# Kernel optimization log

Measured on AMD Instinct MI355X. Metric: run time of the kernel, lower is better.

The kernel has to match this reference:

```python
import jax, jax.numpy as jnp
import numpy as np


def _conv1x1(x, w, b):
    # x: [B, Cin, T, H, W], w: [Cout, Cin], b: [Cout] -> [B, Cout, T, H, W]
    return jnp.einsum('bcthw,oc->bothw', x, w) + b[None, :, None, None, None]


def setup_inputs() -> dict:
    key = jax.random.key(0)
    ks = jax.random.split(key, 9)
    B, Ci, T, H, W = 2, 128, 4, 32, 32
    Co = 64
    s_in = 1.0 / np.sqrt(Ci)
    s_out = 1.0 / np.sqrt(Co)
    return {
        'z': jax.random.normal(ks[0], (B, Ci, T, H, W), dtype=jnp.float32),
        'w_theta': jax.random.uniform(ks[1], (Co, Ci), jnp.float32, -s_in, s_in),
        'b_theta': jax.random.uniform(ks[2], (Co,), jnp.float32, -s_in, s_in),
        'w_phi': jax.random.uniform(ks[3], (Co, Ci), jnp.float32, -s_in, s_in),
        'b_phi': jax.random.uniform(ks[4], (Co,), jnp.float32, -s_in, s_in),
        'w_psi': jax.random.uniform(ks[5], (Co, Ci), jnp.float32, -s_in, s_in),
        'b_psi': jax.random.uniform(ks[6], (Co,), jnp.float32, -s_in, s_in),
        'w_v': jax.random.uniform(ks[7], (Ci, Co), jnp.float32, -s_out, s_out),
        'b_v': jax.random.uniform(ks[8], (Ci,), jnp.float32, -s_out, s_out),
    }


def reference(z, w_theta, b_theta, w_phi, b_phi, w_psi, b_psi, w_v, b_v):
    B, Ci, T, H, W = z.shape
    Co = w_theta.shape[0]
    N = T * H * W
    # 1x1 conv projections, flattened to [B, Co, N]
    theta = _conv1x1(z, w_theta, b_theta).reshape(B, Co, N)
    phi = _conv1x1(z, w_phi, b_phi).reshape(B, Co, N)
    psi = _conv1x1(z, w_psi, b_psi).reshape(B, Co, N)
    # g = phi^T @ psi : [B, N, N]; normalize with ReLU(g / N)
    g = jnp.einsum('bcn,bcm->bnm', phi, psi)
    norm_g = jax.nn.relu(g / jnp.asarray(N, z.dtype))
    # tmp = norm_g @ theta^T -> [B, N, Co] -> [B, Co, T, H, W]
    tmp = jnp.einsum('bnm,bcm->bcn', norm_g, theta).reshape(B, Co, T, H, W)
    vg = _conv1x1(tmp, w_v, b_v)
    return vg + z
```

## Files before the change

### kernel.cpp

```cpp
#include <hip/hip_runtime.h>


#define NSEQ 4096
#define CI 128
#define CO 64

typedef __attribute__((ext_vector_type(8))) short bf16x8;
typedef __attribute__((ext_vector_type(4))) short bf16x4;
typedef __attribute__((ext_vector_type(4))) float f32x4;

static __device__ inline short f2bf(float f) {
  union { float f; unsigned u; } v; v.f = f;
  unsigned r = v.u + 0x7fffu + ((v.u >> 16) & 1u);
  return (short)(r >> 16);
}

__global__ __launch_bounds__(256, 1) void proj_kernel(
    const float* __restrict__ z,
    const float* __restrict__ w_th, const float* __restrict__ b_th,
    const float* __restrict__ w_ph, const float* __restrict__ b_ph,
    const float* __restrict__ w_ps, const float* __restrict__ b_ps,
    short* __restrict__ Qg, short* __restrict__ Kg, short* __restrict__ Vt)
{
  __shared__ f32x4 zt4[16384 / 16];
  char* zt = (char*)zt4;

  const int wgid = blockIdx.x;
  const int b = wgid >> 6;
  const int n0 = (wgid & 63) * 64;
  const int t = threadIdx.x;

  {
    const int ck = t & 15;
    const int cr = t >> 4;
#pragma unroll
    for (int g = 0; g < 8; ++g) {
      const int c = g * 16 + cr;
      f32x4 v = *(const f32x4*)(z + (size_t)(b * CI + c) * NSEQ + n0 + ck * 4);
#pragma unroll
      for (int i = 0; i < 4; ++i) {
        const int n = ck * 4 + i;
        const int chunk = (c >> 3) ^ (n & 7);
        *(short*)(zt + n * 256 + chunk * 16 + (c & 7) * 2) = f2bf(v[i]);
      }
    }
  }
  __syncthreads();

  const int w = t >> 6, l = t & 63, lr = l & 15, lg = l >> 4;
  const int nw = w * 16;
  const f32x4 zero4 = {0.f, 0.f, 0.f, 0.f};

  bf16x8 a[4];
#pragma unroll
  for (int ks = 0; ks < 4; ++ks) {
    const int n = nw + lr;
    const int chunk = (ks * 4 + lg) ^ (n & 7);
    a[ks] = *(const bf16x8*)(zt + n * 256 + chunk * 16);
  }

  const float* Ws[3]   = {w_ph, w_ps, w_th};
  const float* Bias[3] = {b_ph, b_ps, b_th};

#pragma unroll
  for (int mat = 0; mat < 3; ++mat) {
    const float* W = Ws[mat];
#pragma unroll
    for (int osub = 0; osub < 4; ++osub) {
      const int o = osub * 16 + lr;
      f32x4 acc = zero4;
#pragma unroll
      for (int ks = 0; ks < 4; ++ks) {
        const float* wp = W + o * CI + ks * 32 + lg * 8;
        f32x4 x0 = *(const f32x4*)wp;
        f32x4 x1 = *(const f32x4*)(wp + 4);
        bf16x8 bf;
#pragma unroll
        for (int j = 0; j < 4; ++j) { bf[j] = f2bf(x0[j]); bf[4 + j] = f2bf(x1[j]); }
        acc = __builtin_amdgcn_mfma_f32_16x16x32_bf16(a[ks], bf, acc, 0, 0, 0);
      }
      const float bias = Bias[mat][o];
      if (mat == 2) {
        bf16x4 pk;
#pragma unroll
        for (int r = 0; r < 4; ++r) pk[r] = f2bf(acc[r] + bias);
        *(bf16x4*)(Vt + (size_t)(b * CO + o) * NSEQ + n0 + nw + lg * 4) = pk;
      } else {
        short* dst = (mat == 0 ? Qg : Kg) + (size_t)(b * NSEQ + n0 + nw + lg * 4) * CO + o;
#pragma unroll
        for (int r = 0; r < 4; ++r) dst[(size_t)r * CO] = f2bf(acc[r] + bias);
      }
    }
  }
}

__global__ __launch_bounds__(256, 1) void attn_kernel(
    const short* __restrict__ Qg, const short* __restrict__ Kg,
    const short* __restrict__ Vt, const float* __restrict__ w_v,
    const float* __restrict__ b_v, const float* __restrict__ z,
    float* __restrict__ out)
{
  __shared__ f32x4 smem4[40960 / 16];
  char* smem = (char*)smem4;

  const int wg = blockIdx.x;
  const int b = wg >> 7;
  const int nt = wg & 127;
  const int n0 = nt * 32;
  const int t = threadIdx.x;
  const int w = t >> 6;
  const int l = t & 63;
  const int lr = l & 15;
  const int lg = l >> 4;
  const int tw = w >> 1;
  const int nbase = n0 + (w & 1) * 16;
  const f32x4 zero4 = {0.f, 0.f, 0.f, 0.f};

  bf16x8 q0, q1;
  {
    const short* qp = Qg + (size_t)(b * NSEQ + nbase + lr) * CO + lg * 8;
    q0 = *(const bf16x8*)qp;
    q1 = *(const bf16x8*)(qp + 32);
  }

  f32x4 oacc[4];
#pragma unroll
  for (int i = 0; i < 4; ++i) oacc[i] = zero4;

  char* Pb = smem + 32768 + w * 2048;

  bf16x8 stg[8];
  auto load_stage = [&](int ss) {
    const int m0 = ss * 128;
#pragma unroll
    for (int r = 0; r < 8; ++r) {
      const int chunk = r * 256 + w * 64 + l;
      const int row = (chunk >> 3) & 63;
      const int lc = chunk & 7;
      const short* src;
      if (r < 4) {
        const int m = m0 + (chunk >> 9) * 64 + row;
        src = Kg + (size_t)(b * NSEQ + m) * CO + lc * 8;
      } else {
        src = Vt + (size_t)(b * CO + row) * NSEQ + m0 + ((chunk >> 9) - 2) * 64 + lc * 8;
      }
      stg[r] = *(const bf16x8*)src;
    }
  };
  auto write_stage = [&]() {
#pragma unroll
    for (int r = 0; r < 8; ++r) {
      const int chunk = r * 256 + w * 64 + l;
      const int row = (chunk >> 3) & 63;
      const int pc = (chunk & 7) ^ (row & 7);
      *(bf16x8*)(smem + (chunk >> 9) * 8192 + row * 128 + pc * 16) = stg[r];
    }
  };

  load_stage(0);
  write_stage();
  __syncthreads();

  const char* Kt  = smem + tw * 8192;
  const char* Vtl = smem + 16384 + tw * 8192;

  for (int ss = 0; ss < 32; ++ss) {
    if (ss < 31) load_stage(ss + 1);

#pragma unroll
    for (int msub = 0; msub < 4; ++msub) {
      const int m = msub * 16 + lr;
      bf16x8 k0 = *(const bf16x8*)(Kt + m * 128 + ((lg ^ (m & 7)) * 16));
      bf16x8 k1 = *(const bf16x8*)(Kt + m * 128 + (((4 + lg) ^ (m & 7)) * 16));
      f32x4 s = __builtin_amdgcn_mfma_f32_16x16x32_bf16(q0, k0, zero4, 0, 0, 0);
      s = __builtin_amdgcn_mfma_f32_16x16x32_bf16(q1, k1, s, 0, 0, 0);
#pragma unroll
      for (int r = 0; r < 4; ++r) {
        const int nl = lg * 4 + r;
        const int ml = msub * 16 + lr;
        const float p = s[r] > 0.f ? s[r] * (1.f / 4096.f) : 0.f;
        *(short*)(Pb + nl * 128 + ((2 * ml) ^ ((nl & 7) << 4))) = f2bf(p);
      }
    }
    bf16x8 pa0 = *(const bf16x8*)(Pb + lr * 128 + ((lg ^ (lr & 7)) * 16));
    bf16x8 pa1 = *(const bf16x8*)(Pb + lr * 128 + (((4 + lg) ^ (lr & 7)) * 16));
#pragma unroll
    for (int osub = 0; osub < 4; ++osub) {
      const int o = osub * 16 + lr;
      bf16x8 v0 = *(const bf16x8*)(Vtl + o * 128 + ((lg ^ (o & 7)) * 16));
      bf16x8 v1 = *(const bf16x8*)(Vtl + o * 128 + (((4 + lg) ^ (o & 7)) * 16));
      oacc[osub] = __builtin_amdgcn_mfma_f32_16x16x32_bf16(pa0, v0, oacc[osub], 0, 0, 0);
      oacc[osub] = __builtin_amdgcn_mfma_f32_16x16x32_bf16(pa1, v1, oacc[osub], 0, 0, 0);
    }

    __syncthreads();
    if (ss < 31) {
      write_stage();
      __syncthreads();
    }
  }

  float* ored = (float*)smem;
  if (tw == 1) {
    float* dst = ored + (w & 1) * 1024;
#pragma unroll
    for (int osub = 0; osub < 4; ++osub)
#pragma unroll
      for (int r = 0; r < 4; ++r)
        dst[(lg * 4 + r) * 64 + osub * 16 + lr] = oacc[osub][r];
  }
  __syncthreads();

  if (tw == 0) {
    const float* sp = ored + (w & 1) * 1024;
#pragma unroll
    for (int osub = 0; osub < 4; ++osub) {
#pragma unroll
      for (int r = 0; r < 4; ++r) {
        const float v = oacc[osub][r] + sp[(lg * 4 + r) * 64 + osub * 16 + lr];
        const int nl = lg * 4 + r;
        const int ol = osub * 16 + lr;
        *(short*)(Pb + nl * 128 + ((2 * ol) ^ ((nl & 7) << 4))) = f2bf(v);
      }
    }
    bf16x8 oa0 = *(const bf16x8*)(Pb + lr * 128 + ((lg ^ (lr & 7)) * 16));
    bf16x8 oa1 = *(const bf16x8*)(Pb + lr * 128 + (((4 + lg) ^ (lr & 7)) * 16));

#pragma unroll
    for (int cis = 0; cis < 8; ++cis) {
      const int ci = cis * 16 + lr;
      const float* wp = w_v + ci * CO + lg * 8;
      f32x4 wa0 = *(const f32x4*)wp;
      f32x4 wa1 = *(const f32x4*)(wp + 4);
      f32x4 wb0 = *(const f32x4*)(wp + 32);
      f32x4 wb1 = *(const f32x4*)(wp + 36);
      bf16x8 wf0, wf1;
#pragma unroll
      for (int j = 0; j < 4; ++j) {
        wf0[j] = f2bf(wa0[j]); wf0[4 + j] = f2bf(wa1[j]);
        wf1[j] = f2bf(wb0[j]); wf1[4 + j] = f2bf(wb1[j]);
      }
      f32x4 e = __builtin_amdgcn_mfma_f32_16x16x32_bf16(oa0, wf0, zero4, 0, 0, 0);
      e = __builtin_amdgcn_mfma_f32_16x16x32_bf16(oa1, wf1, e, 0, 0, 0);

      const size_t off = (size_t)(b * CI + ci) * NSEQ + nbase + lg * 4;
      f32x4 zv = *(const f32x4*)(z + off);
      const float bias = b_v[ci];
      f32x4 res;
#pragma unroll
      for (int r = 0; r < 4; ++r) res[r] = e[r] + zv[r] + bias;
      *(f32x4*)(out + off) = res;
    }
  }
}

extern "C" void kernel_launch(void* const* d_in, const int* in_sizes, int n_in,
                              void* d_out, int out_size, void* d_ws, size_t ws_size,
                              hipStream_t stream) {
  const float* z    = (const float*)d_in[0];
  const float* w_th = (const float*)d_in[1];
  const float* b_th = (const float*)d_in[2];
  const float* w_ph = (const float*)d_in[3];
  const float* b_ph = (const float*)d_in[4];
  const float* w_ps = (const float*)d_in[5];
  const float* b_ps = (const float*)d_in[6];
  const float* w_v  = (const float*)d_in[7];
  const float* b_v  = (const float*)d_in[8];
  float* out = (float*)d_out;

  short* Qg = (short*)d_ws;
  short* Kg = Qg + 2 * NSEQ * CO;
  short* Vt = Kg + 2 * NSEQ * CO;

  proj_kernel<<<128, 256, 0, stream>>>(z, w_th, b_th, w_ph, b_ph, w_ps, b_ps,
                                       Qg, Kg, Vt);
  attn_kernel<<<256, 256, 0, stream>>>(Qg, Kg, Vt, w_v, b_v, z, out);
}
```

Before: 121.0 us.

## Keep P in registers using transposed MFMA operands, drop LDS P round-trip

The attention loop now computes S transposed (K as the A operand) so each lane's four P values feed a 16x16x16 MFMA directly as the B operand. This removes the per-tile scalar LDS writes and re-reads of P and the extra 8KB of LDS, at the cost of more, smaller MFMAs. The projection kernel is reorganised to reuse converted weight fragments across four n-subtiles and write Q/K with vector stores. The epilogue avoids another LDS transpose but now does scalar out/z accesses per element.

```diff
diff --git a/kernel.cpp b/kernel.cpp
--- a/kernel.cpp
+++ b/kernel.cpp
@@ -14,6 +14,19 @@
   unsigned r = v.u + 0x7fffu + ((v.u >> 16) & 1u);
   return (short)(r >> 16);
 }
+
+#define MFMA32(a, b, c) __builtin_amdgcn_mfma_f32_16x16x32_bf16(a, b, c, 0, 0, 0)
+
+#if __has_builtin(__builtin_amdgcn_mfma_f32_16x16x16bf16_1k)
+static __device__ inline f32x4 mfma16(bf16x4 a, bf16x4 b, f32x4 c) {
+  return __builtin_amdgcn_mfma_f32_16x16x16bf16_1k(a, b, c, 0, 0, 0);
+}
+#else
+static __device__ inline f32x4 mfma16(bf16x4 a, bf16x4 b, f32x4 c) {
+  asm("v_mfma_f32_16x16x16_bf16 %0, %1, %2, %0" : "+v"(c) : "v"(a), "v"(b));
+  return c;
+}
+#endif
 
 __global__ __launch_bounds__(256, 1) void proj_kernel(
     const float* __restrict__ z,
@@ -48,49 +61,68 @@
   __syncthreads();
 
   const int w = t >> 6, l = t & 63, lr = l & 15, lg = l >> 4;
-  const int nw = w * 16;
   const f32x4 zero4 = {0.f, 0.f, 0.f, 0.f};
 
-  bf16x8 a[4];
-#pragma unroll
-  for (int ks = 0; ks < 4; ++ks) {
-    const int n = nw + lr;
-    const int chunk = (ks * 4 + lg) ^ (n & 7);
-    a[ks] = *(const bf16x8*)(zt + n * 256 + chunk * 16);
-  }
-
-  const float* Ws[3]   = {w_ph, w_ps, w_th};
-  const float* Bias[3] = {b_ph, b_ps, b_th};
-
-#pragma unroll
-  for (int mat = 0; mat < 3; ++mat) {
-    const float* W = Ws[mat];
-#pragma unroll
-    for (int osub = 0; osub < 4; ++osub) {
-      const int o = osub * 16 + lr;
-      f32x4 acc = zero4;
+  bf16x8 zf[4][4];
+#pragma unroll
+  for (int nsub = 0; nsub < 4; ++nsub) {
+#pragma unroll
+    for (int ks = 0; ks < 4; ++ks) {
+      const int n = nsub * 16 + lr;
+      const int chunk = (ks * 4 + lg) ^ (n & 7);
+      zf[nsub][ks] = *(const bf16x8*)(zt + n * 256 + chunk * 16);
+    }
+  }
+
+  {
+    const float* Wm[2]   = {w_ph, w_ps};
+    const float* Bm[2]   = {b_ph, b_ps};
+    short*       Dm[2]   = {Qg, Kg};
+#pragma unroll
+    for (int mt = 0; mt < 2; ++mt) {
+      bf16x8 wf[4];
 #pragma unroll
       for (int ks = 0; ks < 4; ++ks) {
-        const float* wp = W + o * CI + ks * 32 + lg * 8;
+        const float* wp = Wm[mt] + (w * 16 + lr) * CI + ks * 32 + lg * 8;
         f32x4 x0 = *(const f32x4*)wp;
         f32x4 x1 = *(const f32x4*)(wp + 4);
-        bf16x8 bf;
-#pragma unroll
-        for (int j = 0; j < 4; ++j) { bf[j] = f2bf(x0[j]); bf[4 + j] = f2bf(x1[j]); }
-        acc = __builtin_amdgcn_mfma_f32_16x16x32_bf16(a[ks], bf, acc, 0, 0, 0);
-      }
-      const float bias = Bias[mat][o];
-      if (mat == 2) {
+#pragma unroll
+        for (int j = 0; j < 4; ++j) { wf[ks][j] = f2bf(x0[j]); wf[ks][4 + j] = f2bf(x1[j]); }
+      }
+      const f32x4 bias4 = *(const f32x4*)(Bm[mt] + w * 16 + lg * 4);
+#pragma unroll
+      for (int nsub = 0; nsub < 4; ++nsub) {
+        f32x4 acc = zero4;
+#pragma unroll
+        for (int ks = 0; ks < 4; ++ks)
+          acc = MFMA32(wf[ks], zf[nsub][ks], acc);
         bf16x4 pk;
 #pragma unroll
-        for (int r = 0; r < 4; ++r) pk[r] = f2bf(acc[r] + bias);
-        *(bf16x4*)(Vt + (size_t)(b * CO + o) * NSEQ + n0 + nw + lg * 4) = pk;
-      } else {
-        short* dst = (mat == 0 ? Qg : Kg) + (size_t)(b * NSEQ + n0 + nw + lg * 4) * CO + o;
-#pragma unroll
-        for (int r = 0; r < 4; ++r) dst[(size_t)r * CO] = f2bf(acc[r] + bias);
-      }
-    }
+        for (int r = 0; r < 4; ++r) pk[r] = f2bf(acc[r] + bias4[r]);
+        *(bf16x4*)(Dm[mt] + (size_t)(b * NSEQ + n0 + nsub * 16 + lr) * CO + w * 16 + lg * 4) = pk;
+      }
+    }
+  }
+
+#pragma unroll
+  for (int osub = 0; osub < 4; ++osub) {
+    f32x4 acc = zero4;
+#pragma unroll
+    for (int ks = 0; ks < 4; ++ks) {
+      const float* wp = w_th + (osub * 16 + lr) * CI + ks * 32 + lg * 8;
+      f32x4 x0 = *(const f32x4*)wp;
+      f32x4 x1 = *(const f32x4*)(wp + 4);
+      bf16x8 wtf;
+#pragma unroll
+      for (int j = 0; j < 4; ++j) { wtf[j] = f2bf(x0[j]); wtf[4 + j] = f2bf(x1[j]); }
+      acc = MFMA32(zf[w][ks], wtf, acc);
+    }
+    const int o = osub * 16 + lr;
+    const float bias = b_th[o];
+    bf16x4 pk;
+#pragma unroll
+    for (int r = 0; r < 4; ++r) pk[r] = f2bf(acc[r] + bias);
+    *(bf16x4*)(Vt + (size_t)(b * CO + o) * NSEQ + n0 + w * 16 + lg * 4) = pk;
   }
 }
 
@@ -100,18 +132,16 @@
     const float* __restrict__ b_v, const float* __restrict__ z,
     float* __restrict__ out)
 {
-  __shared__ f32x4 smem4[40960 / 16];
+  __shared__ f32x4 smem4[32768 / 16];
   char* smem = (char*)smem4;
+  char* Km = smem;
+  char* Vm = smem + 16384;
 
   const int wg = blockIdx.x;
   const int b = wg >> 7;
-  const int nt = wg & 127;
-  const int n0 = nt * 32;
+  const int n0 = (wg & 127) * 32;
   const int t = threadIdx.x;
-  const int w = t >> 6;
-  const int l = t & 63;
-  const int lr = l & 15;
-  const int lg = l >> 4;
+  const int w = t >> 6, l = t & 63, lr = l & 15, lg = l >> 4;
   const int tw = w >> 1;
   const int nbase = n0 + (w & 1) * 16;
   const f32x4 zero4 = {0.f, 0.f, 0.f, 0.f};
@@ -127,33 +157,30 @@
 #pragma unroll
   for (int i = 0; i < 4; ++i) oacc[i] = zero4;
 
-  char* Pb = smem + 32768 + w * 2048;
-
   bf16x8 stg[8];
   auto load_stage = [&](int ss) {
     const int m0 = ss * 128;
 #pragma unroll
-    for (int r = 0; r < 8; ++r) {
-      const int chunk = r * 256 + w * 64 + l;
-      const int row = (chunk >> 3) & 63;
-      const int lc = chunk & 7;
-      const short* src;
-      if (r < 4) {
-        const int m = m0 + (chunk >> 9) * 64 + row;
-        src = Kg + (size_t)(b * NSEQ + m) * CO + lc * 8;
-      } else {
-        src = Vt + (size_t)(b * CO + row) * NSEQ + m0 + ((chunk >> 9) - 2) * 64 + lc * 8;
-      }
-      stg[r] = *(const bf16x8*)src;
+    for (int r = 0; r < 4; ++r) {
+      const int ck = r * 256 + t;
+      stg[r] = *(const bf16x8*)(Kg + (size_t)(b * NSEQ + m0 + (ck >> 3)) * CO + (ck & 7) * 8);
+    }
+#pragma unroll
+    for (int r = 0; r < 4; ++r) {
+      const int cv = r * 256 + t;
+      stg[4 + r] = *(const bf16x8*)(Vt + (size_t)(b * CO + (cv >> 4)) * NSEQ + m0 + (cv & 15) * 8);
     }
   };
   auto write_stage = [&]() {
 #pragma unroll
-    for (int r = 0; r < 8; ++r) {
-      const int chunk = r * 256 + w * 64 + l;
-      const int row = (chunk >> 3) & 63;
-      const int pc = (chunk & 7) ^ (row & 7);
-      *(bf16x8*)(smem + (chunk >> 9) * 8192 + row * 128 + pc * 16) = stg[r];
+    for (int r = 0; r < 4; ++r) {
+      const int ck = r * 256 + t, m = ck >> 3, c8 = ck & 7;
+      *(bf16x8*)(Km + m * 128 + ((c8 ^ (m & 7)) * 16)) = stg[r];
+    }
+#pragma unroll
+    for (int r = 0; r < 4; ++r) {
+      const int cv = r * 256 + t, o = cv >> 4, mc = cv & 15;
+      *(bf16x8*)(Vm + o * 256 + ((mc ^ (o & 7)) * 16)) = stg[4 + r];
     }
   };
 
@@ -161,36 +188,30 @@
   write_stage();
   __syncthreads();
 
-  const char* Kt  = smem + tw * 8192;
-  const char* Vtl = smem + 16384 + tw * 8192;
-
   for (int ss = 0; ss < 32; ++ss) {
     if (ss < 31) load_stage(ss + 1);
 
 #pragma unroll
     for (int msub = 0; msub < 4; ++msub) {
-      const int m = msub * 16 + lr;
-      bf16x8 k0 = *(const bf16x8*)(Kt + m * 128 + ((lg ^ (m & 7)) * 16));
-      bf16x8 k1 = *(const bf16x8*)(Kt + m * 128 + (((4 + lg) ^ (m & 7)) * 16));
-      f32x4 s = __builtin_amdgcn_mfma_f32_16x16x32_bf16(q0, k0, zero4, 0, 0, 0);
-      s = __builtin_amdgcn_mfma_f32_16x16x32_bf16(q1, k1, s, 0, 0, 0);
+      const int mr = tw * 64 + msub * 16 + lr;
+      bf16x8 k0 = *(const bf16x8*)(Km + mr * 128 + ((lg ^ (mr & 7)) * 16));
+      bf16x8 k1 = *(const bf16x8*)(Km + mr * 128 + (((4 + lg) ^ (mr & 7)) * 16));
+      f32x4 s = MFMA32(k0, q0, zero4);
+      s = MFMA32(k1, q1, s);
+      bf16x4 pf;
 #pragma unroll
       for (int r = 0; r < 4; ++r) {
-        const int nl = lg * 4 + r;
-        const int ml = msub * 16 + lr;
         const float p = s[r] > 0.f ? s[r] * (1.f / 4096.f) : 0.f;
-        *(short*)(Pb + nl * 128 + ((2 * ml) ^ ((nl & 7) << 4))) = f2bf(p);
-      }
-    }
-    bf16x8 pa0 = *(const bf16x8*)(Pb + lr * 128 + ((lg ^ (lr & 7)) * 16));
-    bf16x8 pa1 = *(const bf16x8*)(Pb + lr * 128 + (((4 + lg) ^ (lr & 7)) * 16));
-#pragma unroll
-    for (int osub = 0; osub < 4; ++osub) {
-      const int o = osub * 16 + lr;
-      bf16x8 v0 = *(const bf16x8*)(Vtl + o * 128 + ((lg ^ (o & 7)) * 16));
-      bf16x8 v1 = *(const bf16x8*)(Vtl + o * 128 + (((4 + lg) ^ (o & 7)) * 16));
-      oacc[osub] = __builtin_amdgcn_mfma_f32_16x16x32_bf16(pa0, v0, oacc[osub], 0, 0, 0);
-      oacc[osub] = __builtin_amdgcn_mfma_f32_16x16x32_bf16(pa1, v1, oacc[osub], 0, 0, 0);
+        pf[r] = f2bf(p);
+      }
+      const int vchunk = tw * 8 + msub * 2 + (lg >> 1);
+      const int voff = (lg & 1) * 8;
+#pragma unroll
+      for (int osub = 0; osub < 4; ++osub) {
+        const int orow = osub * 16 + lr;
+        bf16x4 vf = *(const bf16x4*)(Vm + orow * 256 + ((vchunk ^ (orow & 7)) * 16) + voff);
+        oacc[osub] = mfma16(vf, pf, oacc[osub]);
+      }
     }
 
     __syncthreads();
@@ -200,56 +221,46 @@
     }
   }
 
-  float* ored = (float*)smem;
+  float* red = (float*)smem;
   if (tw == 1) {
-    float* dst = ored + (w & 1) * 1024;
+    float* dst = red + (w & 1) * 1024;
 #pragma unroll
     for (int osub = 0; osub < 4; ++osub)
 #pragma unroll
       for (int r = 0; r < 4; ++r)
-        dst[(lg * 4 + r) * 64 + osub * 16 + lr] = oacc[osub][r];
+        dst[(osub * 16 + lg * 4 + r) * 16 + lr] = oacc[osub][r];
   }
   __syncthreads();
 
   if (tw == 0) {
-    const float* sp = ored + (w & 1) * 1024;
+    const float* sp = red + (w & 1) * 1024;
+    bf16x4 of[4];
 #pragma unroll
     for (int osub = 0; osub < 4; ++osub) {
 #pragma unroll
       for (int r = 0; r < 4; ++r) {
-        const float v = oacc[osub][r] + sp[(lg * 4 + r) * 64 + osub * 16 + lr];
-        const int nl = lg * 4 + r;
-        const int ol = osub * 16 + lr;
-        *(short*)(Pb + nl * 128 + ((2 * ol) ^ ((nl & 7) << 4))) = f2bf(v);
-      }
-    }
-    bf16x8 oa0 = *(const bf16x8*)(Pb + lr * 128 + ((lg ^ (lr & 7)) * 16));
-    bf16x8 oa1 = *(const bf16x8*)(Pb + lr * 128 + (((4 + lg) ^ (lr & 7)) * 16));
-
+        const float v = oacc[osub][r] + sp[(osub * 16 + lg * 4 + r) * 16 + lr];
+        of[osub][r] = f2bf(v);
+      }
+    }
 #pragma unroll
     for (int cis = 0; cis < 8; ++cis) {
-      const int ci = cis * 16 + lr;
-      const float* wp = w_v + ci * CO + lg * 8;
-      f32x4 wa0 = *(const f32x4*)wp;
-      f32x4 wa1 = *(const f32x4*)(wp + 4);
-      f32x4 wb0 = *(const f32x4*)(wp + 32);
-      f32x4 wb1 = *(const f32x4*)(wp + 36);
-      bf16x8 wf0, wf1;
-#pragma unroll
-      for (int j = 0; j < 4; ++j) {
-        wf0[j] = f2bf(wa0[j]); wf0[4 + j] = f2bf(wa1[j]);
-        wf1[j] = f2bf(wb0[j]); wf1[4 + j] = f2bf(wb1[j]);
-      }
-      f32x4 e = __builtin_amdgcn_mfma_f32_16x16x32_bf16(oa0, wf0, zero4, 0, 0, 0);
-      e = __builtin_amdgcn_mfma_f32_16x16x32_bf16(oa1, wf1, e, 0, 0, 0);
-
-      const size_t off = (size_t)(b * CI + ci) * NSEQ + nbase + lg * 4;
-      f32x4 zv = *(const f32x4*)(z + off);
-      const float bias = b_v[ci];
-      f32x4 res;
-#pragma unroll
-      for (int r = 0; r < 4; ++r) res[r] = e[r] + zv[r] + bias;
-      *(f32x4*)(out + off) = res;
+      f32x4 e = zero4;
+#pragma unroll
+      for (int osub = 0; osub < 4; ++osub) {
+        f32x4 wl = *(const f32x4*)(w_v + (cis * 16 + lr) * CO + osub * 16 + lg * 4);
+        bf16x4 wf;
+#pragma unroll
+        for (int j = 0; j < 4; ++j) wf[j] = f2bf(wl[j]);
+        e = mfma16(wf, of[osub], e);
+      }
+      const f32x4 bv = *(const f32x4*)(b_v + cis * 16 + lg * 4);
+#pragma unroll
+      for (int r = 0; r < 4; ++r) {
+        const int ci = cis * 16 + lg * 4 + r;
+        const size_t off = (size_t)(b * CI + ci) * NSEQ + nbase + lr;
+        out[off] = e[r] + z[off] + bv[r];
+      }
     }
   }
 }
```

Result: slower. 125.8 us (+4.0%).
